# Optimization experiments

Measured on AMD Instinct MI355X. Metric: run time of the kernel, lower is better.

## Reference

```python
import jax, jax.numpy as jnp
import numpy as np

D_MODEL = 1024
NUM_HEADS = 16


def setup_inputs() -> dict:
    key = jax.random.key(0)
    ks = jax.random.split(key, 9)
    B, S, D = 4, 1024, D_MODEL
    scale = 1.0 / np.sqrt(D)
    inp = {
        "query": jax.random.normal(ks[0], (B, S, D), dtype=jnp.float32),
        "key": jax.random.normal(ks[1], (B, S, D), dtype=jnp.float32),
        "value": jax.random.normal(ks[2], (B, S, D), dtype=jnp.float32),
        # causal mask: 1 = attend, 0 = blocked (masked_fill where mask==0)
        "mask": jnp.tril(jnp.ones((S, S), dtype=jnp.int32))[None, None, :, :],
        "Wq": jax.random.normal(ks[3], (D, D), dtype=jnp.float32) * scale,
        "Wk": jax.random.normal(ks[4], (D, D), dtype=jnp.float32) * scale,
        "Wv": jax.random.normal(ks[5], (D, D), dtype=jnp.float32) * scale,
        "Wo": jax.random.normal(ks[6], (D, D), dtype=jnp.float32) * scale,
        "bo": jnp.zeros((D,), dtype=jnp.float32),
    }
    return inp


def reference(query, key, value, mask, Wq, Wk, Wv, Wo, bo):
    B, S, D = query.shape
    H = NUM_HEADS
    dk = D // H
    # torch Linear: y = x @ W.T  (bias=False for q/k/v)
    def proj(x, W):
        return (x @ W.T).reshape(B, S, H, dk).transpose(0, 2, 1, 3)  # [B,H,S,dk]

    Q = proj(query, Wq)
    K = proj(key, Wk)
    V = proj(value, Wv)

    scores = jnp.einsum("bhqd,bhkd->bhqk", Q, K) / jnp.sqrt(
        jnp.asarray(dk, dtype=jnp.float32)
    )
    scores = jnp.where(mask == 0, jnp.asarray(-1e9, scores.dtype), scores)
    attn = jax.nn.softmax(scores, axis=-1)
    out = jnp.einsum("bhqk,bhkd->bhqd", attn, V)  # [B,H,S,dk]
    out = out.transpose(0, 2, 1, 3).reshape(B, S, D)
    return out @ Wo.T + bo
```

## Files before the change

### kernel.cpp

```cpp
#include <hip/hip_runtime.h>

typedef __bf16 bf16x8 __attribute__((ext_vector_type(8)));
typedef short  s16x8  __attribute__((ext_vector_type(8)));
typedef float  f32x4  __attribute__((ext_vector_type(4)));
typedef float  f32x16 __attribute__((ext_vector_type(16)));
typedef unsigned int   u32x4 __attribute__((ext_vector_type(4)));
typedef unsigned short u16x4 __attribute__((ext_vector_type(4)));

#define NH   16
#define HD   64
#define SEQ  1024
#define DM   1024
#define NB   4
#define MTOT 4096

#define SCALE_L2E 0.1803368801111204f

__device__ __forceinline__ unsigned short f2bf(float f) {
    unsigned u = __builtin_bit_cast(unsigned, f);
    u += 0x7FFFu + ((u >> 16) & 1u);
    return (unsigned short)(u >> 16);
}

__device__ __forceinline__ s16x8 cvt8(f32x4 a, f32x4 b) {
    s16x8 r;
    r[0] = (short)f2bf(a[0]); r[1] = (short)f2bf(a[1]);
    r[2] = (short)f2bf(a[2]); r[3] = (short)f2bf(a[3]);
    r[4] = (short)f2bf(b[0]); r[5] = (short)f2bf(b[1]);
    r[6] = (short)f2bf(b[2]); r[7] = (short)f2bf(b[3]);
    return r;
}

__device__ __forceinline__ unsigned short bfbits(float x) {
    __bf16 h = (__bf16)x;
    return __builtin_bit_cast(unsigned short, h);
}
__device__ __forceinline__ float bf2f(unsigned short b) {
    unsigned u = (unsigned)b << 16;
    return __builtin_bit_cast(float, u);
}
__device__ __forceinline__ unsigned pk2(float a, float b) {
    return (unsigned)bfbits(a) | ((unsigned)bfbits(b) << 16);
}

__device__ __forceinline__ void gl16(const void* g, void* l) {
    __builtin_amdgcn_global_load_lds(
        (const __attribute__((address_space(1))) unsigned int*)g,
        (__attribute__((address_space(3))) unsigned int*)l, 16, 0, 0);
}

__device__ __forceinline__ bf16x8 ldfrag(const char* base, int row, int cb) {
    return __builtin_bit_cast(bf16x8,
        *(const s16x8*)(base + row * 128 + (cb ^ ((row & 7) << 4))));
}

__device__ __forceinline__ void loadH512(const float* __restrict__ src, int grow0,
                                         int k0, int tid, f32x4 v[4])
{
    const int row = tid >> 3;
    const int ce  = (tid & 7) * 8;
    const f32x4* p0 = (const f32x4*)(src + (size_t)(grow0 + row) * DM + k0 + ce);
    v[0] = p0[0]; v[1] = p0[1];
    const f32x4* p1 = (const f32x4*)(src + (size_t)(grow0 + 64 + row) * DM + k0 + ce);
    v[2] = p1[0]; v[3] = p1[1];
}
__device__ __forceinline__ void writeH512(char* dst, int tid, const f32x4 v[4], float scl)
{
    const int row = tid >> 3;
    const int cB  = (tid & 7) * 16;
    *(s16x8*)(dst + row * 128 + (cB ^ ((row & 7) << 4))) = cvt8(v[0] * scl, v[1] * scl);
    const int r2 = row + 64;
    *(s16x8*)(dst + r2 * 128 + (cB ^ ((r2 & 7) << 4))) = cvt8(v[2] * scl, v[3] * scl);
}

__device__ __forceinline__ void loadB256(const float* __restrict__ src, int row0,
                                         int k0, int tid, f32x4 v[8])
{
    const int ce = (tid & 7) * 8;
    #pragma unroll
    for (int i = 0; i < 4; ++i) {
        const int row = (tid >> 3) + i * 32;
        const f32x4* p = (const f32x4*)(src + (size_t)(row0 + row) * DM + k0 + ce);
        v[2 * i] = p[0]; v[2 * i + 1] = p[1];
    }
}
__device__ __forceinline__ void writeB256(char* dst, int tid, const f32x4 v[8])
{
    const int cB = (tid & 7) * 16;
    #pragma unroll
    for (int i = 0; i < 4; ++i) {
        const int row = (tid >> 3) + i * 32;
        *(s16x8*)(dst + row * 128 + (cB ^ ((row & 7) << 4))) = cvt8(v[2 * i], v[2 * i + 1]);
    }
}

__device__ __forceinline__ void stage128x64(const unsigned short* __restrict__ src,
                                            int row0, int k0, char* lds, int tid)
{
    const int wv  = tid >> 6;
    const int row = tid >> 3;
    const int scx = ((tid & 7) * 16) ^ ((row & 7) << 4);
    #pragma unroll
    for (int i = 0; i < 4; ++i) {
        const char* g = (const char*)(src + (size_t)(row0 + i * 32 + row) * DM + k0) + scx;
        gl16(g, lds + i * 4096 + wv * 1024);
    }
}

__global__ __launch_bounds__(512, 2)
void proj_kernel(const float* __restrict__ Xq, const float* __restrict__ Xk,
                 const float* __restrict__ Xv, const float* __restrict__ Wq,
                 const float* __restrict__ Wk, const float* __restrict__ Wv,
                 unsigned short* __restrict__ Qo, unsigned short* __restrict__ Ko,
                 unsigned short* __restrict__ VTo)
{
    __shared__ char smem[147456];

    const int bid = blockIdx.x;
    const int swz = (bid & 7) * 24 + (bid >> 3);
    const int which = swz >> 6;
    const int rem   = swz & 63;
    const int m0 = (rem >> 2) * 256, n0 = (rem & 3) * 256;

    const float* X = (which == 0) ? Xq : (which == 1) ? Xk : Xv;
    const float* W = (which == 0) ? Wq : (which == 1) ? Wk : Wv;
    const float wscl = (which == 0) ? SCALE_L2E : 1.0f;

    const int tid = threadIdx.x, lane = tid & 63, wv = tid >> 6;
    const int wrB = (wv >> 2) * 128;
    const int wcB = (wv & 3) * 64;
    const int fr = lane & 15, hi = lane >> 4, r4 = hi * 4;

    f32x4 acc[8][4];
    #pragma unroll
    for (int i = 0; i < 8; ++i)
        #pragma unroll
        for (int j = 0; j < 4; ++j) acc[i][j] = (f32x4){0.f, 0.f, 0.f, 0.f};

    {
        f32x4 v[4];
        loadH512(X, m0,       0, tid, v); writeH512(smem +     0, tid, v, 1.0f);
        loadH512(X, m0 + 128, 0, tid, v); writeH512(smem + 16384, tid, v, 1.0f);
        loadH512(W, n0,       0, tid, v); writeH512(smem + 32768, tid, v, wscl);
        loadH512(W, n0 + 128, 0, tid, v); writeH512(smem + 49152, tid, v, wscl);
    }
    __syncthreads();

    for (int t = 0; t < 16; ++t) {
        const char* Abuf = smem + (t & 1) * 65536;
        const char* Bbuf = Abuf + 32768;
        char* nb = smem + ((t & 1) ^ 1) * 65536;
        const int kn = (t + 1) * 64;

        bf16x8 af[2][4], bf01[2][2], bf23[2][2];
        f32x4 h0[4], h1[4], h2[4], h3[4];

        if (t < 15) loadH512(X, m0, kn, tid, h0);
        #pragma unroll
        for (int ks = 0; ks < 2; ++ks) {
            const int cb = ks * 64 + hi * 16;
            #pragma unroll
            for (int mt = 0; mt < 4; ++mt) af[ks][mt] = ldfrag(Abuf, wrB + mt * 16 + fr, cb);
            #pragma unroll
            for (int nt = 0; nt < 2; ++nt) bf01[ks][nt] = ldfrag(Bbuf, wcB + nt * 16 + fr, cb);
        }
        __builtin_amdgcn_s_setprio(1);
        #pragma unroll
        for (int ks = 0; ks < 2; ++ks)
            #pragma unroll
            for (int mt = 0; mt < 4; ++mt)
                #pragma unroll
                for (int nt = 0; nt < 2; ++nt)
                    acc[mt][nt] = __builtin_amdgcn_mfma_f32_16x16x32_bf16(
                        af[ks][mt], bf01[ks][nt], acc[mt][nt], 0, 0, 0);
        __builtin_amdgcn_s_setprio(0);

        __builtin_amdgcn_s_barrier();
        __builtin_amdgcn_sched_barrier(0);
        #pragma unroll
        for (int ks = 0; ks < 2; ++ks) {
            const int cb = ks * 64 + hi * 16;
            #pragma unroll
            for (int nt = 0; nt < 2; ++nt) bf23[ks][nt] = ldfrag(Bbuf, wcB + 32 + nt * 16 + fr, cb);
        }
        if (t < 15) { loadH512(X, m0 + 128, kn, tid, h1); writeH512(nb, tid, h0, 1.0f); }
        __builtin_amdgcn_s_setprio(1);
        #pragma unroll
        for (int ks = 0; ks < 2; ++ks)
            #pragma unroll
            for (int mt = 0; mt < 4; ++mt)
                #pragma unroll
                for (int nt = 0; nt < 2; ++nt)
                    acc[mt][nt + 2] = __builtin_amdgcn_mfma_f32_16x16x32_bf16(
                        af[ks][mt], bf23[ks][nt], acc[mt][nt + 2], 0, 0, 0);
        __builtin_amdgcn_s_setprio(0);

        __builtin_amdgcn_s_barrier();
        __builtin_amdgcn_sched_barrier(0);
        #pragma unroll
        for (int ks = 0; ks < 2; ++ks) {
            const int cb = ks * 64 + hi * 16;
            #pragma unroll
            for (int mt = 0; mt < 4; ++mt) af[ks][mt] = ldfrag(Abuf, wrB + 64 + mt * 16 + fr, cb);
        }
        if (t < 15) { loadH512(W, n0, kn, tid, h2); writeH512(nb + 16384, tid, h1, 1.0f); }
        __builtin_amdgcn_s_setprio(1);
        #pragma unroll
        for (int ks = 0; ks < 2; ++ks)
            #pragma unroll
            for (int mt = 0; mt < 4; ++mt)
                #pragma unroll
                for (int nt = 0; nt < 2; ++nt)
                    acc[mt + 4][nt] = __builtin_amdgcn_mfma_f32_16x16x32_bf16(
                        af[ks][mt], bf01[ks][nt], acc[mt + 4][nt], 0, 0, 0);
        __builtin_amdgcn_s_setprio(0);

        __builtin_amdgcn_s_barrier();
        __builtin_amdgcn_sched_barrier(0);
        if (t < 15) { loadH512(W, n0 + 128, kn, tid, h3); writeH512(nb + 32768, tid, h2, wscl); }
        __builtin_amdgcn_s_setprio(1);
        #pragma unroll
        for (int ks = 0; ks < 2; ++ks)
            #pragma unroll
            for (int mt = 0; mt < 4; ++mt)
                #pragma unroll
                for (int nt = 0; nt < 2; ++nt)
                    acc[mt + 4][nt + 2] = __builtin_amdgcn_mfma_f32_16x16x32_bf16(
                        af[ks][mt], bf23[ks][nt], acc[mt + 4][nt + 2], 0, 0, 0);
        __builtin_amdgcn_s_setprio(0);
        if (t < 15) writeH512(nb + 49152, tid, h3, wscl);
        asm volatile("s_waitcnt lgkmcnt(0)" ::: "memory");
        __builtin_amdgcn_sched_barrier(0);
        __builtin_amdgcn_s_barrier();
    }

    __syncthreads();

    unsigned short* sE = (unsigned short*)(smem + wv * 18432);
    #pragma unroll
    for (int mt = 0; mt < 8; ++mt)
        #pragma unroll
        for (int nt = 0; nt < 4; ++nt)
            #pragma unroll
            for (int r = 0; r < 4; ++r) {
                const int row = mt * 16 + r4 + r;
                const int col = nt * 16 + fr;
                sE[row * 72 + (col ^ (((row >> 3) & 7) << 3))] = f2bf(acc[mt][nt][r]);
            }
    asm volatile("s_waitcnt lgkmcnt(0)" ::: "memory");

    const int hB    = (n0 + wcB) >> 6;
    const int sbase = m0 + wrB;
    const int bb    = sbase >> 10;
    const int srow0 = sbase & 1023;

    if (which < 2) {
        unsigned short* QK = ((which == 0) ? Qo : Ko)
            + (((size_t)(bb * NH + hB)) * SEQ + srow0) * HD;
        #pragma unroll
        for (int it = 0; it < 16; ++it) {
            const int idx = it * 64 + lane;
            const int row = idx >> 3, c = idx & 7;
            s16x8 v = *(const s16x8*)&sE[row * 72 + ((c ^ ((row >> 3) & 7)) * 8)];
            *(s16x8*)(QK + (size_t)row * HD + c * 8) = v;
        }
    } else {
        const int t0 = srow0 >> 6;
        unsigned short* VD = VTo + (size_t)(bb * NH + hB) * (SEQ * HD)
                                 + (size_t)t0 * 4096;
        #pragma unroll
        for (int it = 0; it < 16; ++it) {
            const int tt = it >> 3, r = it & 7;
            const int sb = tt * 64 + (r >> 1) * 16 + (lane >> 5) * 8;
            const int d  = (lane & 31) + (r & 1) * 32;
            s16x8 v;
            #pragma unroll
            for (int j = 0; j < 8; ++j) {
                const int row = sb + j;
                v[j] = (short)sE[row * 72 + (d ^ (((row >> 3) & 7) << 3))];
            }
            *(s16x8*)(VD + (size_t)(tt * 8 + r) * 512 + lane * 8) = v;
        }
    }
}

__global__ __launch_bounds__(256)
void outproj_kernel(const unsigned short* __restrict__ A,
                    const float* __restrict__ Wo,
                    const float* __restrict__ bo,
                    float* __restrict__ Cout)
{
    const int bid = blockIdx.x;
    const int swz = (bid & 7) * 32 + (bid >> 3);
    const int m0 = (swz >> 3) * 128, n0 = (swz & 7) * 128;

    __shared__ char sA[2][16384];
    __shared__ char sB[2][16384];

    const int tid = threadIdx.x, lane = tid & 63, wv = tid >> 6;
    const int wr = (wv >> 1) * 64, wc = (wv & 1) * 64;
    const int fr = lane & 15, hi = lane >> 4, r4 = hi * 4;

    f32x4 acc[4][4];
    #pragma unroll
    for (int i = 0; i < 4; ++i)
        #pragma unroll
        for (int j = 0; j < 4; ++j) acc[i][j] = (f32x4){0.f, 0.f, 0.f, 0.f};

    f32x4 bv[8];
    loadB256(Wo, n0, 0, tid, bv);
    stage128x64(A, m0, 0, sA[0], tid);
    writeB256(sB[0], tid, bv);
    __syncthreads();

    for (int kt = 0; kt < 16; ++kt) {
        const int cur = kt & 1;
        if (kt < 15) {
            loadB256(Wo, n0, (kt + 1) * 64, tid, bv);
            stage128x64(A, m0, (kt + 1) * 64, sA[cur ^ 1], tid);
            asm volatile("s_waitcnt vmcnt(12)" ::: "memory");
        } else {
            asm volatile("s_waitcnt vmcnt(0)" ::: "memory");
        }
        __builtin_amdgcn_s_barrier();
        __builtin_amdgcn_sched_barrier(0);
        #pragma unroll
        for (int ks = 0; ks < 2; ++ks) {
            const int cb = ks * 64 + hi * 16;
            bf16x8 af[4], bfm[4];
            #pragma unroll
            for (int mt = 0; mt < 4; ++mt)
                af[mt] = ldfrag(sA[cur], wr + mt * 16 + fr, cb);
            #pragma unroll
            for (int nt = 0; nt < 4; ++nt)
                bfm[nt] = ldfrag(sB[cur], wc + nt * 16 + fr, cb);
            #pragma unroll
            for (int mt = 0; mt < 4; ++mt)
                #pragma unroll
                for (int nt = 0; nt < 4; ++nt)
                    acc[mt][nt] = __builtin_amdgcn_mfma_f32_16x16x32_bf16(
                        af[mt], bfm[nt], acc[mt][nt], 0, 0, 0);
        }
        if (kt < 15) writeB256(sB[cur ^ 1], tid, bv);
        asm volatile("s_waitcnt lgkmcnt(0)" ::: "memory");
        __builtin_amdgcn_sched_barrier(0);
        __builtin_amdgcn_s_barrier();
    }

    #pragma unroll
    for (int mt = 0; mt < 4; ++mt)
        #pragma unroll
        for (int nt = 0; nt < 4; ++nt)
            #pragma unroll
            for (int r = 0; r < 4; ++r) {
                int gm = m0 + wr + mt * 16 + r4 + r;
                int gn = n0 + wc + nt * 16 + fr;
                Cout[(size_t)gm * DM + gn] = acc[mt][nt][r] + bo[gn];
            }
}

__device__ __forceinline__ void stageK64(const char* Kc, int t, char* myK, int lane) {
    const int krow8 = lane >> 3;
    const int kcol  = ((lane & 7) * 16) ^ (krow8 << 4);
    const char* kb = Kc + (size_t)t * 8192;
    #pragma unroll
    for (int i = 0; i < 8; ++i)
        gl16(kb + (i * 8 + krow8) * 128 + kcol, myK + i * 1024);
}

__global__ __launch_bounds__(256)
void attn_kernel(const unsigned short* __restrict__ Q,
                 const unsigned short* __restrict__ K,
                 const unsigned short* __restrict__ VT,
                 unsigned short* __restrict__ O)
{
    __shared__ char smem[4][8192];

    const int bid = blockIdx.x;
    const int xcd = bid & 7, idx = bid >> 3;
    const int bh  = xcd * 8 + (idx & 7);
    const int rb  = 15 - (idx >> 3);
    const int tid = threadIdx.x, lane = tid & 63, wv = tid >> 6;
    const int g = wv >> 1, p = wv & 1;
    const int q0w = rb * 64 + g * 32;
    const int ql = lane & 31, hi = lane >> 5;
    const int qg = q0w + ql;
    const int ndiag = q0w >> 6;

    char* myK = smem[wv];

    const unsigned short* Qp = Q + (size_t)bh * SEQ * HD;
    const char* Kc  = (const char*)(K  + (size_t)bh * SEQ * HD);
    const char* Vfc = (const char*)(VT + (size_t)bh * SEQ * HD);

    bf16x8 qf[4];
    #pragma unroll
    for (int s = 0; s < 4; ++s)
        qf[s] = __builtin_bit_cast(bf16x8,
            *(const s16x8*)(Qp + (size_t)qg * HD + s * 16 + hi * 8));

    f32x16 o0, o1;
    #pragma unroll
    for (int i = 0; i < 16; ++i) { o0[i] = 0.f; o1[i] = 0.f; }
    float mrow = -3.0e38f, lrow = 0.f;

    if (p <= ndiag) stageK64(Kc, p, myK, lane);

    for (int t = p; t <= ndiag; t += 2) {
        asm volatile("s_waitcnt vmcnt(0)" ::: "memory");
        __builtin_amdgcn_sched_barrier(0);

        f32x16 s0, s1;
        #pragma unroll
        for (int i = 0; i < 16; ++i) { s0[i] = 0.f; s1[i] = 0.f; }
        #pragma unroll
        for (int s = 0; s < 4; ++s) {
            const int cb = s * 32 + hi * 16;
            bf16x8 k0 = ldfrag(myK, ql, cb);
            bf16x8 k1 = ldfrag(myK, 32 + ql, cb);
            s0 = __builtin_amdgcn_mfma_f32_32x32x16_bf16(k0, qf[s], s0, 0, 0, 0);
            s1 = __builtin_amdgcn_mfma_f32_32x32x16_bf16(k1, qf[s], s1, 0, 0, 0);
        }
        asm volatile("s_waitcnt lgkmcnt(0)" ::: "memory");
        __builtin_amdgcn_sched_barrier(0);

        const char* vb = Vfc + (size_t)t * 8192;
        s16x8 vr[8];
        #pragma unroll
        for (int r = 0; r < 8; ++r)
            vr[r] = *(const s16x8*)(vb + r * 1024 + lane * 16);
        if (t + 2 <= ndiag) stageK64(Kc, t + 2, myK, lane);

        if (t == ndiag) {
            #pragma unroll
            for (int r = 0; r < 16; ++r) {
                const int kl = t * 64 + (r & 3) + 8 * (r >> 2) + 4 * hi;
                s0[r] = (kl      <= qg) ? s0[r] : -3.0e38f;
                s1[r] = (kl + 32 <= qg) ? s1[r] : -3.0e38f;
            }
        }

        float mt = s0[0];
        #pragma unroll
        for (int r = 1; r < 16; ++r) mt = fmaxf(mt, s0[r]);
        #pragma unroll
        for (int r = 0; r < 16; ++r) mt = fmaxf(mt, s1[r]);
        mt = fmaxf(mt, __shfl_xor(mt, 32, 64));

        if (!__all(mt - mrow <= 8.0f)) {
            const float mnew = fmaxf(mrow, mt);
            const float pc = __builtin_amdgcn_exp2f(mrow - mnew);
            mrow = mnew;
            lrow *= pc;
            #pragma unroll
            for (int i = 0; i < 16; ++i) { o0[i] *= pc; o1[i] *= pc; }
        }

        float ts = 0.f;
        #pragma unroll
        for (int r = 0; r < 16; ++r) { s0[r] = __builtin_amdgcn_exp2f(s0[r] - mrow); ts += s0[r]; }
        #pragma unroll
        for (int r = 0; r < 16; ++r) { s1[r] = __builtin_amdgcn_exp2f(s1[r] - mrow); ts += s1[r]; }
        ts += __shfl_xor(ts, 32, 64);
        lrow += ts;

        #pragma unroll
        for (int s = 0; s < 4; ++s) {
            const f32x16 ps = (s < 2) ? s0 : s1;
            const int bse = (s & 1) * 8;
            unsigned w0 = pk2(ps[bse + 0], ps[bse + 1]);
            unsigned w1 = pk2(ps[bse + 2], ps[bse + 3]);
            unsigned w2 = pk2(ps[bse + 4], ps[bse + 5]);
            unsigned w3 = pk2(ps[bse + 6], ps[bse + 7]);
            unsigned x0 = (unsigned)__shfl_xor((int)(hi ? w0 : w2), 32, 64);
            unsigned x1 = (unsigned)__shfl_xor((int)(hi ? w1 : w3), 32, 64);
            u32x4 fw;
            fw[0] = hi ? x0 : w0;
            fw[1] = hi ? x1 : w1;
            fw[2] = hi ? w2 : x0;
            fw[3] = hi ? w3 : x1;
            const bf16x8 pfrag = __builtin_bit_cast(bf16x8, fw);
            o0 = __builtin_amdgcn_mfma_f32_32x32x16_bf16(
                __builtin_bit_cast(bf16x8, vr[2 * s]), pfrag, o0, 0, 0, 0);
            o1 = __builtin_amdgcn_mfma_f32_32x32x16_bf16(
                __builtin_bit_cast(bf16x8, vr[2 * s + 1]), pfrag, o1, 0, 0, 0);
        }
    }

    if (p == 1) {
        unsigned* rec = (unsigned*)smem[wv] + lane * 21;
        #pragma unroll
        for (int i = 0; i < 8; ++i) rec[i]     = pk2(o0[2 * i], o0[2 * i + 1]);
        #pragma unroll
        for (int i = 0; i < 8; ++i) rec[8 + i] = pk2(o1[2 * i], o1[2 * i + 1]);
        rec[16] = __builtin_bit_cast(unsigned, mrow);
        rec[17] = __builtin_bit_cast(unsigned, lrow);
        asm volatile("s_waitcnt lgkmcnt(0)" ::: "memory");
    }
    __syncthreads();
    if (p == 0) {
        const unsigned* rec = (const unsigned*)smem[wv + 1] + lane * 21;
        const float m1 = __builtin_bit_cast(float, rec[16]);
        const float l1 = __builtin_bit_cast(float, rec[17]);
        const float ms = fmaxf(mrow, m1);
        const float c0 = __builtin_amdgcn_exp2f(mrow - ms);
        const float c1 = __builtin_amdgcn_exp2f(m1 - ms);
        const float inv = 1.0f / (lrow * c0 + l1 * c1);
        const float a0 = c0 * inv, a1 = c1 * inv;

        unsigned short* sE = (unsigned short*)smem[wv];
        #pragma unroll
        for (int dt = 0; dt < 2; ++dt) {
            const f32x16 ov = dt ? o1 : o0;
            #pragma unroll
            for (int j = 0; j < 4; ++j) {
                u16x4 w;
                #pragma unroll
                for (int i = 0; i < 4; ++i) {
                    const int ii = 4 * j + i;
                    const unsigned uw = rec[dt * 8 + (ii >> 1)];
                    const float pv = bf2f((unsigned short)((ii & 1) ? (uw >> 16) : (uw & 0xffff)));
                    w[i] = bfbits(ov[ii] * a0 + pv * a1);
                }
                *(u16x4*)&sE[ql * 72 + dt * 32 + 8 * j + 4 * hi] = w;
            }
        }
        asm volatile("s_waitcnt lgkmcnt(0)" ::: "memory");
        const int bb = bh >> 4, h = bh & 15;
        #pragma unroll
        for (int it = 0; it < 4; ++it) {
            const int ix = it * 64 + lane;
            const int qq = ix >> 3, c = ix & 7;
            s16x8 v = *(const s16x8*)&sE[qq * 72 + c * 8];
            *(s16x8*)(O + ((size_t)(bb * SEQ + q0w + qq) * DM + h * 64) + c * 8) = v;
        }
    }
}

extern "C" void kernel_launch(void* const* d_in, const int* in_sizes, int n_in,
                              void* d_out, int out_size, void* d_ws, size_t ws_size,
                              hipStream_t stream)
{
    const float* query = (const float*)d_in[0];
    const float* key   = (const float*)d_in[1];
    const float* value = (const float*)d_in[2];
    const float* Wq = (const float*)d_in[4];
    const float* Wk = (const float*)d_in[5];
    const float* Wv = (const float*)d_in[6];
    const float* Wo = (const float*)d_in[7];
    const float* bo = (const float*)d_in[8];
    float* out = (float*)d_out;

    const size_t XE = (size_t)MTOT * DM;
    unsigned short* ws16 = (unsigned short*)d_ws;
    unsigned short* Qw   = ws16;
    unsigned short* Kw   = Qw + XE;
    unsigned short* VTw  = Kw + XE;
    unsigned short* AO   = VTw + XE;

    proj_kernel<<<dim3(192), dim3(512), 0, stream>>>(
        query, key, value, Wq, Wk, Wv, Qw, Kw, VTw);

    attn_kernel<<<dim3(1024), dim3(256), 0, stream>>>(Qw, Kw, VTw, AO);

    outproj_kernel<<<dim3(256), dim3(256), 0, stream>>>(AO, Wo, bo, out);
}
```

Baseline: 95.81 us.

## Pre-convert projection inputs to bf16 and stage via async global-to-LDS loads

Adds a separate conversion kernel that turns the fp32 Q/K/V activations and weights into bf16 (folding the softmax scale into Wq) in workspace. The projection GEMM then stages tiles with direct global-to-LDS loads instead of loading fp32 into registers, converting, and writing to LDS, with the end-of-iteration barrier moved to the start under a vmcnt wait. This removes register pressure and conversion work from the GEMM inner loop, but adds an extra kernel launch and an extra full read/write pass over about 60 MB of data.

```diff
diff --git a/kernel.cpp b/kernel.cpp
--- a/kernel.cpp
+++ b/kernel.cpp
@@ -54,23 +54,54 @@
         *(const s16x8*)(base + row * 128 + (cb ^ ((row & 7) << 4))));
 }
 
-__device__ __forceinline__ void loadH512(const float* __restrict__ src, int grow0,
-                                         int k0, int tid, f32x4 v[4])
-{
+__global__ __launch_bounds__(256)
+void cvt_kernel(const float* __restrict__ q, const float* __restrict__ k,
+                const float* __restrict__ v, const float* __restrict__ wq,
+                const float* __restrict__ wk, const float* __restrict__ wv,
+                unsigned short* __restrict__ dq, unsigned short* __restrict__ dk,
+                unsigned short* __restrict__ dv, unsigned short* __restrict__ dwq,
+                unsigned short* __restrict__ dwk, unsigned short* __restrict__ dwv)
+{
+    const int id = blockIdx.x;
+    const float* s; unsigned short* d; int off; float scl = 1.0f;
+    if (id < 6144) {
+        const int t = id >> 11; off = id & 2047;
+        s = (t == 0) ? q : (t == 1) ? k : v;
+        d = (t == 0) ? dq : (t == 1) ? dk : dv;
+    } else {
+        const int w = (id - 6144) >> 9; off = (id - 6144) & 511;
+        s = (w == 0) ? wq : (w == 1) ? wk : wv;
+        d = (w == 0) ? dwq : (w == 1) ? dwk : dwv;
+        if (w == 0) scl = SCALE_L2E;
+    }
+    const int idx = off * 2048 + threadIdx.x * 8;
+    const f32x4* sp = (const f32x4*)(s + idx);
+    *(s16x8*)(d + idx) = cvt8(sp[0] * scl, sp[1] * scl);
+}
+
+__device__ __forceinline__ void stage_half(const unsigned short* __restrict__ src,
+                                           int grow0, int k0, char* ldsdst, int tid)
+{
+    const int wv  = tid >> 6;
     const int row = tid >> 3;
-    const int ce  = (tid & 7) * 8;
-    const f32x4* p0 = (const f32x4*)(src + (size_t)(grow0 + row) * DM + k0 + ce);
-    v[0] = p0[0]; v[1] = p0[1];
-    const f32x4* p1 = (const f32x4*)(src + (size_t)(grow0 + 64 + row) * DM + k0 + ce);
-    v[2] = p1[0]; v[3] = p1[1];
-}
-__device__ __forceinline__ void writeH512(char* dst, int tid, const f32x4 v[4], float scl)
-{
+    const int scx = ((tid & 7) * 16) ^ ((row & 7) << 4);
+    gl16((const char*)(src + (size_t)(grow0 + row) * DM + k0) + scx,
+         ldsdst + wv * 1024);
+    gl16((const char*)(src + (size_t)(grow0 + 64 + row) * DM + k0) + scx,
+         ldsdst + 8192 + wv * 1024);
+}
+
+__device__ __forceinline__ void stage128x64(const unsigned short* __restrict__ src,
+                                            int row0, int k0, char* lds, int tid)
+{
+    const int wv  = tid >> 6;
     const int row = tid >> 3;
-    const int cB  = (tid & 7) * 16;
-    *(s16x8*)(dst + row * 128 + (cB ^ ((row & 7) << 4))) = cvt8(v[0] * scl, v[1] * scl);
-    const int r2 = row + 64;
-    *(s16x8*)(dst + r2 * 128 + (cB ^ ((r2 & 7) << 4))) = cvt8(v[2] * scl, v[3] * scl);
+    const int scx = ((tid & 7) * 16) ^ ((row & 7) << 4);
+    #pragma unroll
+    for (int i = 0; i < 4; ++i) {
+        const char* g = (const char*)(src + (size_t)(row0 + i * 32 + row) * DM + k0) + scx;
+        gl16(g, lds + i * 4096 + wv * 1024);
+    }
 }
 
 __device__ __forceinline__ void loadB256(const float* __restrict__ src, int row0,
@@ -94,23 +125,13 @@
     }
 }
 
-__device__ __forceinline__ void stage128x64(const unsigned short* __restrict__ src,
-                                            int row0, int k0, char* lds, int tid)
-{
-    const int wv  = tid >> 6;
-    const int row = tid >> 3;
-    const int scx = ((tid & 7) * 16) ^ ((row & 7) << 4);
-    #pragma unroll
-    for (int i = 0; i < 4; ++i) {
-        const char* g = (const char*)(src + (size_t)(row0 + i * 32 + row) * DM + k0) + scx;
-        gl16(g, lds + i * 4096 + wv * 1024);
-    }
-}
-
 __global__ __launch_bounds__(512, 2)
-void proj_kernel(const float* __restrict__ Xq, const float* __restrict__ Xk,
-                 const float* __restrict__ Xv, const float* __restrict__ Wq,
-                 const float* __restrict__ Wk, const float* __restrict__ Wv,
+void proj_kernel(const unsigned short* __restrict__ Xq,
+                 const unsigned short* __restrict__ Xk,
+                 const unsigned short* __restrict__ Xv,
+                 const unsigned short* __restrict__ Wq,
+                 const unsigned short* __restrict__ Wk,
+                 const unsigned short* __restrict__ Wv,
                  unsigned short* __restrict__ Qo, unsigned short* __restrict__ Ko,
                  unsigned short* __restrict__ VTo)
 {
@@ -122,9 +143,8 @@
     const int rem   = swz & 63;
     const int m0 = (rem >> 2) * 256, n0 = (rem & 3) * 256;
 
-    const float* X = (which == 0) ? Xq : (which == 1) ? Xk : Xv;
-    const float* W = (which == 0) ? Wq : (which == 1) ? Wk : Wv;
-    const float wscl = (which == 0) ? SCALE_L2E : 1.0f;
+    const unsigned short* X = (which == 0) ? Xq : (which == 1) ? Xk : Xv;
+    const unsigned short* W = (which == 0) ? Wq : (which == 1) ? Wk : Wv;
 
     const int tid = threadIdx.x, lane = tid & 63, wv = tid >> 6;
     const int wrB = (wv >> 2) * 128;
@@ -137,14 +157,10 @@
         #pragma unroll
         for (int j = 0; j < 4; ++j) acc[i][j] = (f32x4){0.f, 0.f, 0.f, 0.f};
 
-    {
-        f32x4 v[4];
-        loadH512(X, m0,       0, tid, v); writeH512(smem +     0, tid, v, 1.0f);
-        loadH512(X, m0 + 128, 0, tid, v); writeH512(smem + 16384, tid, v, 1.0f);
-        loadH512(W, n0,       0, tid, v); writeH512(smem + 32768, tid, v, wscl);
-        loadH512(W, n0 + 128, 0, tid, v); writeH512(smem + 49152, tid, v, wscl);
-    }
-    __syncthreads();
+    stage_half(X, m0,       0, smem +     0, tid);
+    stage_half(X, m0 + 128, 0, smem + 16384, tid);
+    stage_half(W, n0,       0, smem + 32768, tid);
+    stage_half(W, n0 + 128, 0, smem + 49152, tid);
 
     for (int t = 0; t < 16; ++t) {
         const char* Abuf = smem + (t & 1) * 65536;
@@ -153,9 +169,15 @@
         const int kn = (t + 1) * 64;
 
         bf16x8 af[2][4], bf01[2][2], bf23[2][2];
-        f32x4 h0[4], h1[4], h2[4], h3[4];
-
-        if (t < 15) loadH512(X, m0, kn, tid, h0);
+
+        if (t < 15) {
+            stage_half(X, m0, kn, nb, tid);
+            asm volatile("s_waitcnt vmcnt(2)" ::: "memory");
+        } else {
+            asm volatile("s_waitcnt vmcnt(0)" ::: "memory");
+        }
+        __builtin_amdgcn_s_barrier();
+        __builtin_amdgcn_sched_barrier(0);
         #pragma unroll
         for (int ks = 0; ks < 2; ++ks) {
             const int cb = ks * 64 + hi * 16;
@@ -183,7 +205,7 @@
             #pragma unroll
             for (int nt = 0; nt < 2; ++nt) bf23[ks][nt] = ldfrag(Bbuf, wcB + 32 + nt * 16 + fr, cb);
         }
-        if (t < 15) { loadH512(X, m0 + 128, kn, tid, h1); writeH512(nb, tid, h0, 1.0f); }
+        if (t < 15) stage_half(X, m0 + 128, kn, nb + 16384, tid);
         __builtin_amdgcn_s_setprio(1);
         #pragma unroll
         for (int ks = 0; ks < 2; ++ks)
@@ -203,7 +225,7 @@
             #pragma unroll
             for (int mt = 0; mt < 4; ++mt) af[ks][mt] = ldfrag(Abuf, wrB + 64 + mt * 16 + fr, cb);
         }
-        if (t < 15) { loadH512(W, n0, kn, tid, h2); writeH512(nb + 16384, tid, h1, 1.0f); }
+        if (t < 15) stage_half(W, n0, kn, nb + 32768, tid);
         __builtin_amdgcn_s_setprio(1);
         #pragma unroll
         for (int ks = 0; ks < 2; ++ks)
@@ -217,7 +239,7 @@
 
         __builtin_amdgcn_s_barrier();
         __builtin_amdgcn_sched_barrier(0);
-        if (t < 15) { loadH512(W, n0 + 128, kn, tid, h3); writeH512(nb + 32768, tid, h2, wscl); }
+        if (t < 15) stage_half(W, n0 + 128, kn, nb + 49152, tid);
         __builtin_amdgcn_s_setprio(1);
         #pragma unroll
         for (int ks = 0; ks < 2; ++ks)
@@ -228,10 +250,6 @@
                     acc[mt + 4][nt + 2] = __builtin_amdgcn_mfma_f32_16x16x32_bf16(
                         af[ks][mt], bf23[ks][nt], acc[mt + 4][nt + 2], 0, 0, 0);
         __builtin_amdgcn_s_setprio(0);
-        if (t < 15) writeH512(nb + 49152, tid, h3, wscl);
-        asm volatile("s_waitcnt lgkmcnt(0)" ::: "memory");
-        __builtin_amdgcn_sched_barrier(0);
-        __builtin_amdgcn_s_barrier();
     }
 
     __syncthreads();
@@ -552,14 +570,25 @@
     float* out = (float*)d_out;
 
     const size_t XE = (size_t)MTOT * DM;
+    const size_t WE = (size_t)DM * DM;
     unsigned short* ws16 = (unsigned short*)d_ws;
-    unsigned short* Qw   = ws16;
+    unsigned short* Xq16 = ws16;
+    unsigned short* Xk16 = Xq16 + XE;
+    unsigned short* Xv16 = Xk16 + XE;
+    unsigned short* Wq16 = Xv16 + XE;
+    unsigned short* Wk16 = Wq16 + WE;
+    unsigned short* Wv16 = Wk16 + WE;
+    unsigned short* Qw   = Wv16 + WE;
     unsigned short* Kw   = Qw + XE;
     unsigned short* VTw  = Kw + XE;
     unsigned short* AO   = VTw + XE;
 
+    cvt_kernel<<<dim3(7680), dim3(256), 0, stream>>>(
+        query, key, value, Wq, Wk, Wv,
+        Xq16, Xk16, Xv16, Wq16, Wk16, Wv16);
+
     proj_kernel<<<dim3(192), dim3(512), 0, stream>>>(
-        query, key, value, Wq, Wk, Wv, Qw, Kw, VTw);
+        Xq16, Xk16, Xv16, Wq16, Wk16, Wv16, Qw, Kw, VTw);
 
     attn_kernel<<<dim3(1024), dim3(256), 0, stream>>>(Qw, Kw, VTw, AO);
 
```

Result: slower. 98.18 us (+2.5%).
